# Kernel optimization log

Measured on AMD Instinct MI355X. Metric: run time of the kernel, lower is better.

## Reference

```python
import jax, jax.numpy as jnp
import numpy as np

NUM_HEAD = 12
HEAD_SIZE = 64


def _rope_sincos(seq_len, dim, dtype):
    # standard sinusoidal rotary tables, repeat-interleaved to full dim
    pos = jnp.arange(seq_len, dtype=jnp.float32)                      # (S,)
    inv_freq = 10000.0 ** (-jnp.arange(0, dim, 2, dtype=jnp.float32) / dim)  # (d/2,)
    ang = pos[:, None] * inv_freq[None, :]                            # (S, d/2)
    sin = jnp.repeat(jnp.sin(ang), 2, axis=-1).astype(dtype)          # (S, d)
    cos = jnp.repeat(jnp.cos(ang), 2, axis=-1).astype(dtype)          # (S, d)
    return sin, cos


def _apply_rope(x, sin, cos):
    # x: (B, S, H, d); rotate interleaved pairs along last dim
    x2 = jnp.stack([-x[..., 1::2], x[..., 0::2]], axis=-1).reshape(x.shape)
    return x * cos[None, :, None, :] + x2 * sin[None, :, None, :]


def setup_inputs() -> dict:
    key = jax.random.key(0)
    k1, k2, k3 = jax.random.split(key, 3)
    B, S, IN = 8, 1024, 768
    OUT = NUM_HEAD * HEAD_SIZE * 2
    input_ = jax.random.normal(k1, (B, S, IN), dtype=jnp.float32)
    W = jax.random.normal(k2, (IN, OUT), dtype=jnp.float32) * 0.02
    b = jax.random.normal(k3, (OUT,), dtype=jnp.float32) * 0.02
    return {"input_": input_, "W": W, "b": b}


def reference(input_, W, b):
    B, S, _ = input_.shape
    hidden = input_ @ W + b                                   # (B, S, H*2d)
    hidden = hidden.reshape(B, S, NUM_HEAD, 2 * HEAD_SIZE)    # split+stack over heads
    qw = hidden[..., :HEAD_SIZE]                              # (B, S, H, d)
    kw = hidden[..., HEAD_SIZE:]
    sin, cos = _rope_sincos(S, HEAD_SIZE, input_.dtype)
    qw = _apply_rope(qw, sin, cos)
    kw = _apply_rope(kw, sin, cos)
    logits = jnp.einsum('bmhd,bnhd->bhmn', qw, kw)            # (B, H, S, S)
    return logits / (NUM_HEAD ** 0.5)
```

## Files before the change

kernel.cpp:

```cpp
#include <hip/hip_runtime.h>
#include <hip/hip_bf16.h>

#define NHEAD 12
#define HSZ   64
#define BATCH 8
#define SEQ   1024
#define KDIM  768
#define NDIM  1536

using f32x4  = __attribute__((ext_vector_type(4))) float;
using bf16x8 = __attribute__((ext_vector_type(8))) __bf16;
typedef unsigned int u32;

__device__ __forceinline__ unsigned short f2bf(float f) {
    unsigned int u = __builtin_bit_cast(unsigned int, f);
    u += 0x7fffu + ((u >> 16) & 1u);
    return (unsigned short)(u >> 16);
}

__device__ __forceinline__ void gl_lds16(const unsigned short* g, unsigned short* l) {
    __builtin_amdgcn_global_load_lds(
        (const __attribute__((address_space(1))) u32*)g,
        (__attribute__((address_space(3))) u32*)l, 16, 0, 0);
}

__device__ __forceinline__ int swz16(int row, int c16) { return (c16 ^ (row & 7)); }

#define NCONV 3072
#define NTRAN 1152
#define NTAB  128
__global__ __launch_bounds__(256) void prep(
        const float* __restrict__ input, const float* __restrict__ W,
        unsigned short* __restrict__ Abf, unsigned short* __restrict__ Wt,
        float2* __restrict__ tab) {
    __shared__ unsigned short tl[32][33];
    const int b = blockIdx.x, t = threadIdx.x;
    if (b < NCONV) {
        const size_t base = ((size_t)b * 256 + t) * 8;
        const f32x4 v0 = *reinterpret_cast<const f32x4*>(input + base);
        const f32x4 v1 = *reinterpret_cast<const f32x4*>(input + base + 4);
        uint4 o;
        o.x = (u32)f2bf(v0[0]) | ((u32)f2bf(v0[1]) << 16);
        o.y = (u32)f2bf(v0[2]) | ((u32)f2bf(v0[3]) << 16);
        o.z = (u32)f2bf(v1[0]) | ((u32)f2bf(v1[1]) << 16);
        o.w = (u32)f2bf(v1[2]) | ((u32)f2bf(v1[3]) << 16);
        *reinterpret_cast<uint4*>(Abf + base) = o;
    } else if (b < NCONV + NTRAN) {
        const int tb = b - NCONV;
        const int n0 = (tb % 48) * 32, k0 = (tb / 48) * 32;
        const int tx = t & 31, ty = t >> 5;
#pragma unroll
        for (int r = 0; r < 4; ++r)
            tl[ty + r * 8][tx] = f2bf(W[(size_t)(k0 + ty + r * 8) * NDIM + n0 + tx]);
        __syncthreads();
#pragma unroll
        for (int r = 0; r < 4; ++r)
            Wt[(size_t)(n0 + ty + r * 8) * KDIM + k0 + tx] = tl[tx][ty + r * 8];
    } else {
        const int idx = (b - NCONV - NTRAN) * 256 + t;
        const int s = idx >> 5, i = idx & 31;
        const float inv = exp2f(-(float)i * (13.287712379549449f / 32.0f));
        const float ang = (float)s * inv;
        tab[idx] = make_float2(sinf(ang), cosf(ang));
    }
}

__global__ __launch_bounds__(512, 6) void gemm1_rope(
        const unsigned short* __restrict__ Abf, const unsigned short* __restrict__ Wt,
        const float* __restrict__ bias, const float2* __restrict__ tab,
        unsigned short* __restrict__ qws, unsigned short* __restrict__ kws) {
    __shared__ unsigned short As[128 * 64];
    __shared__ unsigned short Bs[128 * 64];
    const int t  = threadIdx.x;
    const int flat = blockIdx.x;
    const int id = (flat & 7) * 96 + (flat >> 3);
    const int mt = id / 12, nt = id % 12;
    const int m0 = mt * 128, n0 = nt * 128;
    const int lane = t & 63, wid = t >> 6;
    const int wm = wid >> 2, wn = wid & 3;
    const int lr = lane & 15, lg = lane >> 4;
    const int lr8 = lane >> 3;
    const int src8 = ((lane & 7) ^ lr8) * 8;

    f32x4 acc[4][2] = {};
    char* asb = reinterpret_cast<char*>(As);
    char* bsb = reinterpret_cast<char*>(Bs);

    for (int kt = 0; kt < KDIM / 64; ++kt) {
        if (kt) __syncthreads();
        const int kbase = kt * 64;
#pragma unroll
        for (int p = 0; p < 2; ++p) {
            const int rb = wid * 16 + p * 8;
            gl_lds16(Abf + (size_t)(m0 + rb + lr8) * KDIM + kbase + src8, As + rb * 64);
            gl_lds16(Wt  + (size_t)(n0 + rb + lr8) * KDIM + kbase + src8, Bs + rb * 64);
        }
        __syncthreads();
#pragma unroll
        for (int kk = 0; kk < 2; ++kk) {
            bf16x8 a[4], b[2];
#pragma unroll
            for (int mf = 0; mf < 4; ++mf) {
                const int r = wm * 64 + mf * 16 + lr;
                a[mf] = *reinterpret_cast<const bf16x8*>(asb + r * 128 + swz16(r, kk * 4 + lg) * 16);
            }
#pragma unroll
            for (int nf = 0; nf < 2; ++nf) {
                const int r = wn * 32 + nf * 16 + lr;
                b[nf] = *reinterpret_cast<const bf16x8*>(bsb + r * 128 + swz16(r, kk * 4 + lg) * 16);
            }
#pragma unroll
            for (int mf = 0; mf < 4; ++mf)
#pragma unroll
                for (int nf = 0; nf < 2; ++nf)
                    acc[mf][nf] = __builtin_amdgcn_mfma_f32_16x16x32_bf16(
                        a[mf], b[nf], acc[mf][nf], 0, 0, 0);
        }
    }

    float bv[2];
#pragma unroll
    for (int nf = 0; nf < 2; ++nf) bv[nf] = bias[n0 + wn * 32 + nf * 16 + lr];
    const int h = nt;
    unsigned short* outw = (wn < 2) ? qws : kws;
    const float oscale = (wn < 2) ? 0.28867513459481287f : 1.0f;
#pragma unroll
    for (int nf = 0; nf < 2; ++nf) {
        const int d = (wn * 32 + nf * 16 + lr) & 63;
        const int i = d >> 1;
        const float sgn = (d & 1) ? 1.0f : -1.0f;
#pragma unroll
        for (int mf = 0; mf < 4; ++mf) {
#pragma unroll
            for (int r = 0; r < 4; ++r) {
                const int m = m0 + wm * 64 + mf * 16 + lg * 4 + r;
                const float v = acc[mf][nf][r] + bv[nf];
                const float p = __shfl_xor(v, 1, 64);
                const int s = m & (SEQ - 1), b_ = m >> 10;
                const float2 sc = tab[s * 32 + i];
                const float o = (v * sc.y + sgn * p * sc.x) * oscale;
                outw[(size_t)(((b_ * NHEAD + h) * SEQ + s) * HSZ) + d] = f2bf(o);
            }
        }
    }
}

__global__ __launch_bounds__(256) void qk_logits(
        const unsigned short* __restrict__ qws, const unsigned short* __restrict__ kws,
        float* __restrict__ out) {
    __shared__ __align__(16) char smem[32768];
    unsigned short* Qs = reinterpret_cast<unsigned short*>(smem);
    unsigned short* Ks = reinterpret_cast<unsigned short*>(smem + 16384);
    const int t = threadIdx.x;
    const int flat = blockIdx.x;
    const int id = (flat & 7) * 768 + (flat >> 3);
    const int bh = id >> 6, tile = id & 63;
    const int tm = tile >> 3, tn = tile & 7;
    const int m0 = tm * 128, n0 = tn * 128;
    const unsigned short* Qb = qws + (size_t)bh * SEQ * HSZ;
    const unsigned short* Kb = kws + (size_t)bh * SEQ * HSZ;
    const int lane = t & 63, wid = t >> 6;
    const int lr8 = lane >> 3;
    const int src8 = ((lane & 7) ^ lr8) * 8;
#pragma unroll
    for (int p = 0; p < 4; ++p) {
        const int rb = wid * 32 + p * 8;
        gl_lds16(Qb + (size_t)(m0 + rb + lr8) * HSZ + src8, Qs + rb * 64);
        gl_lds16(Kb + (size_t)(n0 + rb + lr8) * HSZ + src8, Ks + rb * 64);
    }
    __syncthreads();
    const int wm = wid >> 1, wn = wid & 1;
    const int lr = lane & 15, lg = lane >> 4;
    char* qsb = smem;
    char* ksb = smem + 16384;
    f32x4 acc[4][4] = {};
#pragma unroll
    for (int kk = 0; kk < 2; ++kk) {
        bf16x8 a[4], b[4];
#pragma unroll
        for (int mf = 0; mf < 4; ++mf) {
            const int r = wm * 64 + mf * 16 + lr;
            a[mf] = *reinterpret_cast<const bf16x8*>(qsb + r * 128 + swz16(r, kk * 4 + lg) * 16);
        }
#pragma unroll
        for (int nf = 0; nf < 4; ++nf) {
            const int r = wn * 64 + nf * 16 + lr;
            b[nf] = *reinterpret_cast<const bf16x8*>(ksb + r * 128 + swz16(r, kk * 4 + lg) * 16);
        }
#pragma unroll
        for (int mf = 0; mf < 4; ++mf)
#pragma unroll
            for (int nf = 0; nf < 4; ++nf)
                acc[mf][nf] = __builtin_amdgcn_mfma_f32_16x16x32_bf16(
                    a[mf], b[nf], acc[mf][nf], 0, 0, 0);
    }
    float* ob = out + (size_t)bh * SEQ * SEQ;
#pragma unroll
    for (int c = 0; c < 2; ++c) {
        __syncthreads();
        if (wm == c) {
#pragma unroll
            for (int mf = 0; mf < 4; ++mf) {
#pragma unroll
                for (int nf = 0; nf < 4; ++nf) {
                    const int nc = wn * 64 + nf * 16 + lr;
                    const int b16 = nc >> 2;
#pragma unroll
                    for (int r = 0; r < 4; ++r) {
                        const int ml = mf * 16 + lg * 4 + r;
                        const int sb = (b16 & 24) | ((b16 & 7) ^ (ml & 7));
                        *reinterpret_cast<float*>(smem + ml * 512 + sb * 16 + (nc & 3) * 4)
                            = acc[mf][nf][r];
                    }
                }
            }
        }
        __syncthreads();
#pragma unroll
        for (int it = 0; it < 8; ++it) {
            const int fl = it * 256 + t;
            const int ml = fl >> 5;
            const int b = fl & 31;
            const int sb = (b & 24) | ((b & 7) ^ (ml & 7));
            const f32x4 v = *reinterpret_cast<const f32x4*>(smem + ml * 512 + sb * 16);
            __builtin_nontemporal_store(v,
                reinterpret_cast<f32x4*>(ob + (size_t)(m0 + c * 64 + ml) * SEQ + n0 + b * 4));
        }
    }
}

extern "C" void kernel_launch(void* const* d_in, const int* in_sizes, int n_in,
                              void* d_out, int out_size, void* d_ws, size_t ws_size,
                              hipStream_t stream) {
    const float* input = (const float*)d_in[0];
    const float* W     = (const float*)d_in[1];
    const float* bias  = (const float*)d_in[2];
    float* out = (float*)d_out;

    const size_t QK_ELEMS = (size_t)BATCH * NHEAD * SEQ * HSZ;
    unsigned short* qws = (unsigned short*)d_ws;
    unsigned short* kws = qws + QK_ELEMS;
    unsigned short* Wt  = kws + QK_ELEMS;
    unsigned short* Abf = Wt + (size_t)NDIM * KDIM;
    float2* tab = (float2*)(Abf + (size_t)BATCH * SEQ * KDIM);

    hipLaunchKernelGGL(prep, dim3(NCONV + NTRAN + NTAB), dim3(256), 0, stream,
                       input, W, Abf, Wt, tab);
    hipLaunchKernelGGL(gemm1_rope, dim3(768), dim3(512), 0, stream,
                       Abf, Wt, bias, tab, qws, kws);
    hipLaunchKernelGGL(qk_logits, dim3(96 * 64), dim3(256), 0, stream, qws, kws, out);
}
```

Before: 109.2 us.

## Double-buffer LDS tiles in projection GEMM with prefetch of next K slice

After: 113.6 us. +4.0%, slower.

```diff
diff --git a/kernel.cpp b/kernel.cpp
--- a/kernel.cpp
+++ b/kernel.cpp
@@ -69,8 +69,8 @@
         const unsigned short* __restrict__ Abf, const unsigned short* __restrict__ Wt,
         const float* __restrict__ bias, const float2* __restrict__ tab,
         unsigned short* __restrict__ qws, unsigned short* __restrict__ kws) {
-    __shared__ unsigned short As[128 * 64];
-    __shared__ unsigned short Bs[128 * 64];
+    __shared__ unsigned short As[2][128 * 32];
+    __shared__ unsigned short Bs[2][128 * 32];
     const int t  = threadIdx.x;
     const int flat = blockIdx.x;
     const int id = (flat & 7) * 96 + (flat >> 3);
@@ -79,43 +79,42 @@
     const int lane = t & 63, wid = t >> 6;
     const int wm = wid >> 2, wn = wid & 3;
     const int lr = lane & 15, lg = lane >> 4;
-    const int lr8 = lane >> 3;
-    const int src8 = ((lane & 7) ^ lr8) * 8;
+    const int srow = wid * 16 + (lane >> 2);
+    const int soff = (((lane & 3) ^ ((lane >> 2) & 3)) * 8);
 
     f32x4 acc[4][2] = {};
-    char* asb = reinterpret_cast<char*>(As);
-    char* bsb = reinterpret_cast<char*>(Bs);
-
-    for (int kt = 0; kt < KDIM / 64; ++kt) {
-        if (kt) __syncthreads();
-        const int kbase = kt * 64;
-#pragma unroll
-        for (int p = 0; p < 2; ++p) {
-            const int rb = wid * 16 + p * 8;
-            gl_lds16(Abf + (size_t)(m0 + rb + lr8) * KDIM + kbase + src8, As + rb * 64);
-            gl_lds16(Wt  + (size_t)(n0 + rb + lr8) * KDIM + kbase + src8, Bs + rb * 64);
-        }
-        __syncthreads();
-#pragma unroll
-        for (int kk = 0; kk < 2; ++kk) {
-            bf16x8 a[4], b[2];
-#pragma unroll
-            for (int mf = 0; mf < 4; ++mf) {
-                const int r = wm * 64 + mf * 16 + lr;
-                a[mf] = *reinterpret_cast<const bf16x8*>(asb + r * 128 + swz16(r, kk * 4 + lg) * 16);
-            }
-#pragma unroll
-            for (int nf = 0; nf < 2; ++nf) {
-                const int r = wn * 32 + nf * 16 + lr;
-                b[nf] = *reinterpret_cast<const bf16x8*>(bsb + r * 128 + swz16(r, kk * 4 + lg) * 16);
-            }
-#pragma unroll
-            for (int mf = 0; mf < 4; ++mf)
-#pragma unroll
-                for (int nf = 0; nf < 2; ++nf)
-                    acc[mf][nf] = __builtin_amdgcn_mfma_f32_16x16x32_bf16(
-                        a[mf], b[nf], acc[mf][nf], 0, 0, 0);
-        }
+
+    gl_lds16(Abf + (size_t)(m0 + srow) * KDIM + soff, &As[0][wid * 16 * 32]);
+    gl_lds16(Wt  + (size_t)(n0 + srow) * KDIM + soff, &Bs[0][wid * 16 * 32]);
+    __syncthreads();
+
+    for (int kt = 0; kt < KDIM / 32; ++kt) {
+        const int cur = kt & 1;
+        if (kt < KDIM / 32 - 1) {
+            const int kbase = (kt + 1) * 32;
+            gl_lds16(Abf + (size_t)(m0 + srow) * KDIM + kbase + soff, &As[cur ^ 1][wid * 16 * 32]);
+            gl_lds16(Wt  + (size_t)(n0 + srow) * KDIM + kbase + soff, &Bs[cur ^ 1][wid * 16 * 32]);
+        }
+        const char* ac = reinterpret_cast<const char*>(&As[cur][0]);
+        const char* bc = reinterpret_cast<const char*>(&Bs[cur][0]);
+        bf16x8 a[4], b[2];
+#pragma unroll
+        for (int mf = 0; mf < 4; ++mf) {
+            const int r = wm * 64 + mf * 16 + lr;
+            a[mf] = *reinterpret_cast<const bf16x8*>(ac + r * 64 + ((lg ^ (r & 3)) * 16));
+        }
+#pragma unroll
+        for (int nf = 0; nf < 2; ++nf) {
+            const int r = wn * 32 + nf * 16 + lr;
+            b[nf] = *reinterpret_cast<const bf16x8*>(bc + r * 64 + ((lg ^ (r & 3)) * 16));
+        }
+#pragma unroll
+        for (int mf = 0; mf < 4; ++mf)
+#pragma unroll
+            for (int nf = 0; nf < 2; ++nf)
+                acc[mf][nf] = __builtin_amdgcn_mfma_f32_16x16x32_bf16(
+                    a[mf], b[nf], acc[mf][nf], 0, 0, 0);
+        __syncthreads();
     }
 
     float bv[2];
```
